# Performance work log

Measured on AMD Instinct MI355X. Metric: run time of the kernel, lower is better.

## Reference

```python
import jax, jax.numpy as jnp
import numpy as np

NUM_HEADS = 16
R_MIN = 16
R_MAX = 64


def setup_inputs() -> dict:
    key = jax.random.key(0)
    ks = jax.random.split(key, 12)
    bs, S, H = 4, 2048, 1024
    hidden_states = jax.random.normal(ks[0], (bs, S, H), dtype=jnp.float32)
    # Linear layers: y = x @ W.T + b (torch convention, W is [out, in])
    wscale = 1.0 / np.sqrt(H)
    Wq = jax.random.normal(ks[1], (H, H), dtype=jnp.float32) * wscale
    bq = jnp.zeros((H,), dtype=jnp.float32)
    Wk = jax.random.normal(ks[2], (H, H), dtype=jnp.float32) * wscale
    bk = jnp.zeros((H,), dtype=jnp.float32)
    Wv = jax.random.normal(ks[3], (H, H), dtype=jnp.float32) * wscale
    bv = jnp.zeros((H,), dtype=jnp.float32)
    Wo = jax.random.normal(ks[4], (H, H), dtype=jnp.float32) * wscale
    bo = jnp.zeros((H,), dtype=jnp.float32)
    # xavier_uniform for proj_k/proj_v over last two dims (seq_len, r_max)
    xs = float(np.sqrt(6.0 / (S + R_MAX)))
    proj_k = jax.random.uniform(ks[5], (NUM_HEADS, S, R_MAX), dtype=jnp.float32, minval=-xs, maxval=xs)
    proj_v = jax.random.uniform(ks[6], (NUM_HEADS, S, R_MAX), dtype=jnp.float32, minval=-xs, maxval=xs)
    return {
        'hidden_states': hidden_states,
        'Wq': Wq, 'bq': bq, 'Wk': Wk, 'bk': bk, 'Wv': Wv, 'bv': bv,
        'Wo': Wo, 'bo': bo, 'proj_k': proj_k, 'proj_v': proj_v,
    }


def reference(hidden_states, Wq, bq, Wk, bk, Wv, bv, Wo, bo, proj_k, proj_v):
    bs, S, H = hidden_states.shape
    nh = NUM_HEADS
    hd = H // nh

    def heads(x):  # [b,s,H] -> [b,h,s,d]
        return x.reshape(bs, S, nh, hd).transpose(0, 2, 1, 3)

    q = heads(hidden_states @ Wq.T + bq)
    k = heads(hidden_states @ Wk.T + bk)
    v = heads(hidden_states @ Wv.T + bv)

    # dynamic rank from per-sample variance (torch .var is unbiased -> ddof=1)
    batch_var = jnp.var(hidden_states.reshape(bs, -1), axis=1, ddof=1)
    var_norm = (batch_var - batch_var.min()) / (batch_var.max() - batch_var.min() + 1e-6)
    curr_r = jnp.round(R_MIN + var_norm.mean() * (R_MAX - R_MIN)).astype(jnp.int32)

    # low-rank projection of K/V along sequence; compute full r_max, mask at softmax
    key_proj = jnp.einsum('bhld,hlk->bhkd', k, proj_k)      # [b,h,R,d]
    value_proj = jnp.einsum('bhld,hlk->bhkd', v, proj_v)    # [b,h,R,d]

    scores = jnp.einsum('bhsd,bhkd->bhsk', q, key_proj) / jnp.sqrt(jnp.float32(hd))
    rank_mask = jnp.arange(R_MAX) < curr_r                  # [R]
    scores = jnp.where(rank_mask, scores, -jnp.inf)
    attn_probs = jax.nn.softmax(scores, axis=-1)            # zeros beyond curr_r
    # dropout is identity in eval mode
    context = jnp.einsum('bhsk,bhkd->bhsd', attn_probs, value_proj)
    context = context.transpose(0, 2, 1, 3).reshape(bs, S, H)
    output = context @ Wo.T + bo
    return output, attn_probs, curr_r
```

## Files before the change

kernel.cpp:

```cpp
#include <hip/hip_runtime.h>


typedef unsigned short u16;
typedef short s16x8 __attribute__((ext_vector_type(8)));
typedef unsigned short u16x8 __attribute__((ext_vector_type(8)));
typedef float f32x4 __attribute__((ext_vector_type(4)));

#define GLL16(gp, lp) __builtin_amdgcn_global_load_lds( \
    (const __attribute__((address_space(1))) void*)(gp), \
    (__attribute__((address_space(3))) void*)(lp), 16, 0, 0)

__device__ __forceinline__ u16 f2bf(float f) {
    unsigned u = __float_as_uint(f);
    u += 0x7fffu + ((u >> 16) & 1u);
    return (u16)(u >> 16);
}

__device__ __forceinline__ f32x4 mfma16(s16x8 a, s16x8 b, f32x4 c) {
    return __builtin_amdgcn_mfma_f32_16x16x32_bf16(a, b, c, 0, 0, 0);
}

__global__ __launch_bounds__(256) void cast_hs_var_k(const float* __restrict__ hs,
        u16* __restrict__ out, double* __restrict__ red) {
    int t = threadIdx.x;
    size_t base = (size_t)blockIdx.x * 8192;
    double s = 0.0, s2 = 0.0;
    #pragma unroll
    for (int i = 0; i < 4; ++i) {
        size_t idx = base + (size_t)i * 2048 + (size_t)t * 8;
        float4 a = *(const float4*)(hs + idx);
        float4 c = *(const float4*)(hs + idx + 4);
        s  += (double)a.x + (double)a.y + (double)a.z + (double)a.w
            + (double)c.x + (double)c.y + (double)c.z + (double)c.w;
        s2 += (double)a.x * a.x + (double)a.y * a.y + (double)a.z * a.z + (double)a.w * a.w
            + (double)c.x * c.x + (double)c.y * c.y + (double)c.z * c.z + (double)c.w * c.w;
        u16x8 o;
        o[0] = f2bf(a.x); o[1] = f2bf(a.y); o[2] = f2bf(a.z); o[3] = f2bf(a.w);
        o[4] = f2bf(c.x); o[5] = f2bf(c.y); o[6] = f2bf(c.z); o[7] = f2bf(c.w);
        *(u16x8*)(out + idx) = o;
    }
    __shared__ double sa[256], sb[256];
    sa[t] = s; sb[t] = s2;
    __syncthreads();
    for (int o = 128; o > 0; o >>= 1) {
        if (t < o) { sa[t] += sa[t + o]; sb[t] += sb[t + o]; }
        __syncthreads();
    }
    if (t == 0) { red[blockIdx.x * 2] = sa[0]; red[blockIdx.x * 2 + 1] = sb[0]; }
}

__global__ __launch_bounds__(256) void compute_r_k(const double* __restrict__ red,
        int* __restrict__ currp, float* __restrict__ outr) {
    int t = threadIdx.x, lane = t & 63, b = t >> 6;
    double s = 0.0, s2 = 0.0;
    #pragma unroll
    for (int j = 0; j < 4; ++j) {
        int idx = b * 256 + j * 64 + lane;
        s += red[idx * 2]; s2 += red[idx * 2 + 1];
    }
    #pragma unroll
    for (int o = 1; o < 64; o <<= 1) { s += __shfl_xor(s, o); s2 += __shfl_xor(s2, o); }
    __shared__ double vs[4];
    if (lane == 0) {
        const double N = 2097152.0;
        vs[b] = (s2 - s * s / N) / (N - 1.0);
    }
    __syncthreads();
    if (t == 0) {
        double mn = vs[0], mx = vs[0];
        for (int i = 1; i < 4; ++i) { mn = fmin(mn, vs[i]); mx = fmax(mx, vs[i]); }
        double mean = 0.0;
        for (int i = 0; i < 4; ++i) mean += (vs[i] - mn) / (mx - mn + 1e-6);
        mean *= 0.25;
        double r = rint(16.0 + mean * 48.0);
        *currp = (int)r;
        *outr = (float)r;
    }
}

__global__ __launch_bounds__(256) void prep_k(const float* __restrict__ w0,
        const float* __restrict__ w1, const float* __restrict__ w2,
        const float* __restrict__ w3, u16* __restrict__ wout,
        const float* __restrict__ p0, const float* __restrict__ p1,
        u16* __restrict__ q0, u16* __restrict__ q1,
        const float* __restrict__ bq, const float* __restrict__ bk,
        const float* __restrict__ bv, float* __restrict__ biascat) {
    __shared__ float tl[64][65];
    int bid = blockIdx.x, t = threadIdx.x;
    if (bid < 2048) {
        int mat = bid >> 9;
        int off = ((bid & 511) * 256 + t) * 8;
        const float* src = (mat == 0) ? w0 : (mat == 1) ? w1 : (mat == 2) ? w2 : w3;
        float4 a = *(const float4*)(src + off);
        float4 c = *(const float4*)(src + off + 4);
        u16x8 o;
        o[0] = f2bf(a.x); o[1] = f2bf(a.y); o[2] = f2bf(a.z); o[3] = f2bf(a.w);
        o[4] = f2bf(c.x); o[5] = f2bf(c.y); o[6] = f2bf(c.z); o[7] = f2bf(c.w);
        *(u16x8*)(wout + (size_t)mat * 1048576 + off) = o;
    } else if (bid < 3072) {
        int bid2 = bid - 2048;
        int which = bid2 >> 9, bi = bid2 & 511;
        const float* p = which ? p1 : p0;
        u16* pt = which ? q1 : q0;
        int h = bi >> 5, lb = bi & 31;
        {
            int l = t >> 2, r0 = (t & 3) * 16;
            const float* src = p + ((size_t)(h * 2048 + lb * 64 + l)) * 64 + r0;
            #pragma unroll
            for (int u = 0; u < 4; ++u) {
                float4 v = *(const float4*)(src + u * 4);
                tl[l][r0 + u * 4 + 0] = v.x; tl[l][r0 + u * 4 + 1] = v.y;
                tl[l][r0 + u * 4 + 2] = v.z; tl[l][r0 + u * 4 + 3] = v.w;
            }
        }
        __syncthreads();
        {
            int r = t >> 2, l0 = (t & 3) * 16;
            u16x8 o0, o1;
            #pragma unroll
            for (int j = 0; j < 8; ++j) { o0[j] = f2bf(tl[l0 + j][r]); o1[j] = f2bf(tl[l0 + 8 + j][r]); }
            u16* dst = pt + ((size_t)(h * 64 + r)) * 2048 + lb * 64 + l0;
            *(u16x8*)dst = o0;
            *(u16x8*)(dst + 8) = o1;
        }
    } else {
        for (int i = t; i < 3072; i += 256) {
            float v = (i < 1024) ? bq[i] : (i < 2048) ? bk[i - 1024] : bv[i - 2048];
            biascat[i] = v;
        }
    }
}

__global__ __launch_bounds__(512, 2) void qkv_gemm_k(const u16* __restrict__ Ag,
        const u16* __restrict__ Wcat, const float* __restrict__ biascat,
        u16* __restrict__ C) {
    __shared__ u16 lds[40960];
    int bid = blockIdx.x;
    int swz = (bid & 7) * 32 + (bid >> 3);
    int bm = swz >> 3, bn = swz & 7;
    int t = threadIdx.x, lane = t & 63, w = t >> 6, wr = w >> 2, wc = w & 3;

    int srow = w * 16 + (lane >> 2);
    int slog = (((lane & 3) ^ ((lane >> 3) & 3)) << 3);
    const u16* asrc0 = Ag + (size_t)(bm * 256 + srow) * 1024 + slog;
    const u16* bsrc0 = Wcat + (size_t)(bn * 384 + srow) * 1024 + slog;

#define STAGEA(kts, h) GLL16(asrc0 + (h) * 131072 + (kts) * 32, \
                             &lds[(((kts) & 1) * 8192) + (h) * 4096 + w * 512])
#define STAGEB(kts, h) GLL16(bsrc0 + (h) * 131072 + (kts) * 32, \
                             &lds[16384 + (((kts) & 1) * 12288) + (h) * 4096 + w * 512])

    int pcol = (((lane >> 4) ^ (((lane & 15) >> 1) & 3)) << 3);
    int arow0 = (wr * 128 + (lane & 15)) * 32 + pcol;
    int brow0 = 16384 + (wc * 96 + (lane & 15)) * 32 + pcol;

    f32x4 zero4 = {0.f, 0.f, 0.f, 0.f};
    f32x4 acc[8][6];
    #pragma unroll
    for (int m = 0; m < 8; ++m)
        #pragma unroll
        for (int n = 0; n < 6; ++n) acc[m][n] = zero4;

    STAGEA(0, 0); STAGEA(0, 1); STAGEB(0, 0); STAGEB(0, 1); STAGEB(0, 2);
    STAGEA(1, 0); STAGEA(1, 1);
    asm volatile("s_waitcnt vmcnt(2)" ::: "memory");
    __builtin_amdgcn_s_barrier();
    asm volatile("" ::: "memory");

    for (int kt = 0; kt < 32; ++kt) {
        int abase = (kt & 1) * 8192 + arow0;
        int bbase = (kt & 1) * 12288 + brow0;
        s16x8 af[8], bf0, bf1, bf2;

        #pragma unroll
        for (int m = 0; m < 8; ++m) af[m] = *(const s16x8*)&lds[abase + m * 512];
        bf0 = *(const s16x8*)&lds[bbase];
        bf1 = *(const s16x8*)&lds[bbase + 512];
        bf2 = *(const s16x8*)&lds[bbase + 1024];
        if (kt < 31) { STAGEB(kt + 1, 0); STAGEB(kt + 1, 1); STAGEB(kt + 1, 2); }
        asm volatile("s_waitcnt lgkmcnt(0)" ::: "memory");
        __builtin_amdgcn_s_barrier();
        __builtin_amdgcn_s_setprio(1);
        #pragma unroll
        for (int m = 0; m < 8; ++m) {
            acc[m][0] = mfma16(af[m], bf0, acc[m][0]);
            acc[m][1] = mfma16(af[m], bf1, acc[m][1]);
            acc[m][2] = mfma16(af[m], bf2, acc[m][2]);
        }
        __builtin_amdgcn_s_setprio(0);
        __builtin_amdgcn_s_barrier();
        asm volatile("" ::: "memory");

        bf0 = *(const s16x8*)&lds[bbase + 1536];
        bf1 = *(const s16x8*)&lds[bbase + 2048];
        bf2 = *(const s16x8*)&lds[bbase + 2560];
        if (kt < 30) { STAGEA(kt + 2, 0); STAGEA(kt + 2, 1); }
        if (kt < 30) { asm volatile("s_waitcnt vmcnt(2)" ::: "memory"); }
        else if (kt == 30) { asm volatile("s_waitcnt vmcnt(0)" ::: "memory"); }
        asm volatile("s_waitcnt lgkmcnt(0)" ::: "memory");
        __builtin_amdgcn_s_barrier();
        __builtin_amdgcn_s_setprio(1);
        #pragma unroll
        for (int m = 0; m < 8; ++m) {
            acc[m][3] = mfma16(af[m], bf0, acc[m][3]);
            acc[m][4] = mfma16(af[m], bf1, acc[m][4]);
            acc[m][5] = mfma16(af[m], bf2, acc[m][5]);
        }
        __builtin_amdgcn_s_setprio(0);
        __builtin_amdgcn_s_barrier();
        asm volatile("" ::: "memory");
    }

    float bias[6];
    #pragma unroll
    for (int n = 0; n < 6; ++n)
        bias[n] = biascat[bn * 384 + wc * 96 + n * 16 + (lane & 15)];
    #pragma unroll
    for (int m = 0; m < 8; ++m) {
        int row0 = bm * 256 + wr * 128 + m * 16 + ((lane >> 4) << 2);
        #pragma unroll
        for (int n = 0; n < 6; ++n) {
            int col = bn * 384 + wc * 96 + n * 16 + (lane & 15);
            #pragma unroll
            for (int v = 0; v < 4; ++v)
                C[(size_t)(row0 + v) * 3072 + col] = f2bf(acc[m][n][v] + bias[n]);
        }
    }
#undef STAGEA
#undef STAGEB
}

__global__ __launch_bounds__(512, 2) void out_gemm_k(const u16* __restrict__ Ag,
        const u16* __restrict__ Bg, const float* __restrict__ biasg,
        float* __restrict__ Cg) {
    __shared__ u16 lds[24576];
    int bid = blockIdx.x;
    int swz = (bid & 7) * 32 + (bid >> 3);
    int bm = swz >> 3, bn = swz & 7;
    int t = threadIdx.x, lane = t & 63, w = t >> 6, wr = w >> 1, wc = w & 1;

    int srow = w * 16 + (lane >> 2);
    int slog = (((lane & 3) ^ ((lane >> 3) & 3)) << 3);
    const u16* asrc0 = Ag + (size_t)(bm * 256 + srow) * 1024 + slog;
    const u16* bsrc0 = Bg + (size_t)(bn * 128 + srow) * 1024 + slog;

#define STAGEA(kts, h) GLL16(asrc0 + (h) * 131072 + (kts) * 32, \
                             &lds[(((kts) & 1) * 8192) + (h) * 4096 + w * 512])
#define STAGEB(kts) GLL16(bsrc0 + (kts) * 32, \
                          &lds[16384 + (((kts) & 1) * 4096) + w * 512])

    int pcol = (((lane >> 4) ^ (((lane & 15) >> 1) & 3)) << 3);
    int arow0 = (wr * 64 + (lane & 15)) * 32 + pcol;
    int brow0 = 16384 + (wc * 64 + (lane & 15)) * 32 + pcol;

    f32x4 zero4 = {0.f, 0.f, 0.f, 0.f};
    f32x4 acc[4][4];
    #pragma unroll
    for (int m = 0; m < 4; ++m)
        #pragma unroll
        for (int n = 0; n < 4; ++n) acc[m][n] = zero4;

    STAGEA(0, 0); STAGEA(0, 1); STAGEB(0);
    STAGEA(1, 0); STAGEA(1, 1);
    asm volatile("s_waitcnt vmcnt(2)" ::: "memory");
    __builtin_amdgcn_s_barrier();
    asm volatile("" ::: "memory");

    for (int kt = 0; kt < 32; ++kt) {
        int abase = (kt & 1) * 8192 + arow0;
        int bbase = (kt & 1) * 4096 + brow0;
        s16x8 af[4], bf0, bf1;

        #pragma unroll
        for (int m = 0; m < 4; ++m) af[m] = *(const s16x8*)&lds[abase + m * 512];
        bf0 = *(const s16x8*)&lds[bbase];
        bf1 = *(const s16x8*)&lds[bbase + 512];
        if (kt < 31) STAGEB(kt + 1);
        asm volatile("s_waitcnt lgkmcnt(0)" ::: "memory");
        __builtin_amdgcn_s_barrier();
        __builtin_amdgcn_s_setprio(1);
        #pragma unroll
        for (int m = 0; m < 4; ++m) {
            acc[m][0] = mfma16(af[m], bf0, acc[m][0]);
            acc[m][1] = mfma16(af[m], bf1, acc[m][1]);
        }
        __builtin_amdgcn_s_setprio(0);
        __builtin_amdgcn_s_barrier();
        asm volatile("" ::: "memory");

        bf0 = *(const s16x8*)&lds[bbase + 1024];
        bf1 = *(const s16x8*)&lds[bbase + 1536];
        if (kt < 30) { STAGEA(kt + 2, 0); STAGEA(kt + 2, 1); }
        if (kt < 30) { asm volatile("s_waitcnt vmcnt(2)" ::: "memory"); }
        else if (kt == 30) { asm volatile("s_waitcnt vmcnt(0)" ::: "memory"); }
        asm volatile("s_waitcnt lgkmcnt(0)" ::: "memory");
        __builtin_amdgcn_s_barrier();
        __builtin_amdgcn_s_setprio(1);
        #pragma unroll
        for (int m = 0; m < 4; ++m) {
            acc[m][2] = mfma16(af[m], bf0, acc[m][2]);
            acc[m][3] = mfma16(af[m], bf1, acc[m][3]);
        }
        __builtin_amdgcn_s_setprio(0);
        __builtin_amdgcn_s_barrier();
        asm volatile("" ::: "memory");
    }

    float bias[4];
    #pragma unroll
    for (int n = 0; n < 4; ++n)
        bias[n] = biasg[bn * 128 + wc * 64 + n * 16 + (lane & 15)];
    #pragma unroll
    for (int m = 0; m < 4; ++m) {
        int row0 = bm * 256 + wr * 64 + m * 16 + ((lane >> 4) << 2);
        #pragma unroll
        for (int n = 0; n < 4; ++n) {
            int col = bn * 128 + wc * 64 + n * 16 + (lane & 15);
            #pragma unroll
            for (int v = 0; v < 4; ++v)
                Cg[(size_t)(row0 + v) * 1024 + col] = acc[m][n][v] + bias[n];
        }
    }
#undef STAGEA
#undef STAGEB
}

__global__ __launch_bounds__(256) void proj_einsum_k(const u16* __restrict__ qkv,
        const u16* __restrict__ pt0, const u16* __restrict__ pt1,
        float* __restrict__ out0, float* __restrict__ out1) {
    __shared__ u16 kt[256 * 66];
    int c = blockIdx.x, h = blockIdx.y, z = blockIdx.z;
    int which = z >> 2, b = z & 3;
    const u16* kv = qkv + 1024 + which * 1024;
    const u16* pt = which ? pt1 : pt0;
    float* outp = which ? out1 : out0;
    int t = threadIdx.x, lane = t & 63, w = t >> 6;

    int tl = t >> 3, sd = (t & 7) * 8;
    const u16* kvp = kv + (size_t)(b * 2048 + c * 256 + tl) * 3072 + h * 64 + sd;
    s16x8 g[8];
    #pragma unroll
    for (int i = 0; i < 8; ++i) g[i] = *(const s16x8*)(kvp + (size_t)i * 98304);
    #pragma unroll
    for (int i = 0; i < 8; ++i) *(s16x8*)&kt[(tl + 32 * i) * 66 + sd] = g[i];
    __syncthreads();

    f32x4 zero4 = {0.f, 0.f, 0.f, 0.f};
    f32x4 acc[4] = {zero4, zero4, zero4, zero4};
    const u16* ptb_ = pt + (size_t)(h * 64 + (lane & 15)) * 2048 + c * 256 + ((lane >> 4) << 3);
    int gcol = w * 16 + (lane & 15);
    int gk0 = (lane >> 4) << 3;

    #pragma unroll
    for (int ks = 0; ks < 8; ++ks) {
        s16x8 bf;
        int kb = (ks * 32 + gk0) * 66 + gcol;
        #pragma unroll
        for (int j = 0; j < 8; ++j) bf[j] = (short)kt[kb + j * 66];
        #pragma unroll
        for (int m = 0; m < 4; ++m) {
            s16x8 af = *(const s16x8*)(ptb_ + (size_t)m * 32768 + ks * 32);
            acc[m] = mfma16(af, bf, acc[m]);
        }
    }

    float* ob = outp + (size_t)((c * 4 + b) * 16 + h) * 4096;
    #pragma unroll
    for (int m = 0; m < 4; ++m)
        #pragma unroll
        for (int v = 0; v < 4; ++v)
            ob[(m * 16 + ((lane >> 4) << 2) + v) * 64 + w * 16 + (lane & 15)] = acc[m][v];
}

__global__ __launch_bounds__(256) void reduce_kv_k(const float* __restrict__ kp_part,
        const float* __restrict__ vp_part, u16* __restrict__ kpb, u16* __restrict__ vpb) {
    int h = blockIdx.x, b = blockIdx.y, t = threadIdx.x;
    int base = (b * 16 + h) * 4096 + t * 16;
    float4 zf = {0.f, 0.f, 0.f, 0.f};
    float4 sk[4] = {zf, zf, zf, zf}, sv[4] = {zf, zf, zf, zf};
    #pragma unroll
    for (int c = 0; c < 8; ++c) {
        #pragma unroll
        for (int u = 0; u < 4; ++u) {
            float4 a = *(const float4*)&kp_part[c * 262144 + base + u * 4];
            float4 g = *(const float4*)&vp_part[c * 262144 + base + u * 4];
            sk[u].x += a.x; sk[u].y += a.y; sk[u].z += a.z; sk[u].w += a.w;
            sv[u].x += g.x; sv[u].y += g.y; sv[u].z += g.z; sv[u].w += g.w;
        }
    }
    int r = t >> 2, d0 = (t & 3) * 16;
    size_t ob = (size_t)(b * 16 + h) * 4096;
    u16x8 o0, o1;
    o0[0] = f2bf(sk[0].x); o0[1] = f2bf(sk[0].y); o0[2] = f2bf(sk[0].z); o0[3] = f2bf(sk[0].w);
    o0[4] = f2bf(sk[1].x); o0[5] = f2bf(sk[1].y); o0[6] = f2bf(sk[1].z); o0[7] = f2bf(sk[1].w);
    o1[0] = f2bf(sk[2].x); o1[1] = f2bf(sk[2].y); o1[2] = f2bf(sk[2].z); o1[3] = f2bf(sk[2].w);
    o1[4] = f2bf(sk[3].x); o1[5] = f2bf(sk[3].y); o1[6] = f2bf(sk[3].z); o1[7] = f2bf(sk[3].w);
    *(u16x8*)&kpb[ob + r * 64 + d0]     = o0;
    *(u16x8*)&kpb[ob + r * 64 + d0 + 8] = o1;
    #pragma unroll
    for (int u = 0; u < 4; ++u) {
        int d = d0 + u * 4;
        vpb[ob + (size_t)(d + 0) * 64 + r] = f2bf(sv[u].x);
        vpb[ob + (size_t)(d + 1) * 64 + r] = f2bf(sv[u].y);
        vpb[ob + (size_t)(d + 2) * 64 + r] = f2bf(sv[u].z);
        vpb[ob + (size_t)(d + 3) * 64 + r] = f2bf(sv[u].w);
    }
}

__global__ __launch_bounds__(256) void attn_k(const u16* __restrict__ qkv,
        const u16* __restrict__ kpb, const u16* __restrict__ vpb,
        const int* __restrict__ currp, float* __restrict__ probs, u16* __restrict__ ctxb) {
    int sb = blockIdx.x, h = blockIdx.y, b = blockIdx.z;
    int cr = *currp;
    __shared__ u16 kpl[64 * 80];
    __shared__ u16 vpl[64 * 80];
    __shared__ u16 pl[64 * 80];
    int t = threadIdx.x, lane = t & 63, w = t >> 6;

    {
        int r = t >> 2, d0 = (t & 3) * 16;
        size_t ob = (size_t)(b * 16 + h) * 4096 + t * 16;
        u16x8 k0 = *(const u16x8*)(kpb + ob), k1 = *(const u16x8*)(kpb + ob + 8);
        u16x8 v0 = *(const u16x8*)(vpb + ob), v1 = *(const u16x8*)(vpb + ob + 8);
        *(u16x8*)&kpl[r * 80 + d0]     = k0;
        *(u16x8*)&kpl[r * 80 + d0 + 8] = k1;
        *(u16x8*)&vpl[r * 80 + d0]     = v0;
        *(u16x8*)&vpl[r * 80 + d0 + 8] = v1;
    }
    __syncthreads();

    const u16* qp = qkv + (size_t)(b * 2048 + sb * 64 + w * 16 + (lane & 15)) * 3072 + h * 64 + ((lane >> 4) << 3);
    s16x8 q0 = *(const s16x8*)qp;
    s16x8 q1 = *(const s16x8*)(qp + 32);
    f32x4 zero4 = {0.f, 0.f, 0.f, 0.f};
    f32x4 sc[4];
    #pragma unroll
    for (int j = 0; j < 4; ++j) {
        sc[j] = zero4;
        s16x8 k0 = *(const s16x8*)&kpl[(j * 16 + (lane & 15)) * 80 + ((lane >> 4) << 3)];
        s16x8 k1 = *(const s16x8*)&kpl[(j * 16 + (lane & 15)) * 80 + 32 + ((lane >> 4) << 3)];
        sc[j] = mfma16(q0, k0, sc[j]);
        sc[j] = mfma16(q1, k1, sc[j]);
    }

    const float scale = 0.125f;
    float p_[4][4];
    #pragma unroll
    for (int v = 0; v < 4; ++v) {
        float m = -3.0e38f;
        #pragma unroll
        for (int j = 0; j < 4; ++j) {
            int rr = j * 16 + (lane & 15);
            if (rr < cr) m = fmaxf(m, sc[j][v] * scale);
        }
        m = fmaxf(m, __shfl_xor(m, 1));
        m = fmaxf(m, __shfl_xor(m, 2));
        m = fmaxf(m, __shfl_xor(m, 4));
        m = fmaxf(m, __shfl_xor(m, 8));
        float s = 0.f;
        #pragma unroll
        for (int j = 0; j < 4; ++j) {
            int rr = j * 16 + (lane & 15);
            float p = (rr < cr) ? __expf(sc[j][v] * scale - m) : 0.f;
            p_[j][v] = p; s += p;
        }
        s += __shfl_xor(s, 1); s += __shfl_xor(s, 2);
        s += __shfl_xor(s, 4); s += __shfl_xor(s, 8);
        float inv = 1.f / s;
        #pragma unroll
        for (int j = 0; j < 4; ++j) p_[j][v] *= inv;
    }

    int srow = w * 16 + ((lane >> 4) << 2);
    #pragma unroll
    for (int v = 0; v < 4; ++v) {
        int sg = sb * 64 + srow + v;
        #pragma unroll
        for (int j = 0; j < 4; ++j) {
            int rr = j * 16 + (lane & 15);
            probs[(size_t)((b * 16 + h) * 2048 + sg) * 64 + rr] = p_[j][v];
            pl[(srow + v) * 80 + rr] = f2bf(p_[j][v]);
        }
    }
    __syncthreads();

    f32x4 co[4] = {zero4, zero4, zero4, zero4};
    #pragma unroll
    for (int ks = 0; ks < 2; ++ks) {
        s16x8 pa = *(const s16x8*)&pl[(w * 16 + (lane & 15)) * 80 + ks * 32 + ((lane >> 4) << 3)];
        #pragma unroll
        for (int n = 0; n < 4; ++n) {
            s16x8 vf = *(const s16x8*)&vpl[(n * 16 + (lane & 15)) * 80 + ks * 32 + ((lane >> 4) << 3)];
            co[n] = mfma16(pa, vf, co[n]);
        }
    }
    #pragma unroll
    for (int n = 0; n < 4; ++n)
        #pragma unroll
        for (int v = 0; v < 4; ++v)
            ctxb[(size_t)((b * 2048 + sb * 64 + srow + v) * 16 + h) * 64 + n * 16 + (lane & 15)] = f2bf(co[n][v]);
}

extern "C" void kernel_launch(void* const* d_in, const int* in_sizes, int n_in,
                              void* d_out, int out_size, void* d_ws, size_t ws_size,
                              hipStream_t stream) {
    const float* hs = (const float*)d_in[0];
    const float* Wq = (const float*)d_in[1];
    const float* bq = (const float*)d_in[2];
    const float* Wk = (const float*)d_in[3];
    const float* bk = (const float*)d_in[4];
    const float* Wv = (const float*)d_in[5];
    const float* bv = (const float*)d_in[6];
    const float* Wo = (const float*)d_in[7];
    const float* bo = (const float*)d_in[8];
    const float* pk = (const float*)d_in[9];
    const float* pv = (const float*)d_in[10];
    float* out = (float*)d_out;
    char* w = (char*)d_ws;

    u16* hsb   = (u16*)(w + 0);
    float* vp_part = (float*)(w + 0);
    u16* ctxb  = (u16*)(w + 0);
    u16* wqb   = (u16*)(w + 16777216);
    u16* ptb   = (u16*)(w + 25165824);
    u16* pvtb  = (u16*)(w + 29360128);
    u16* qkvb  = (u16*)(w + 33554432);
    float* kp_part = (float*)(w + 83886080);
    float* biascat = (float*)(w + 92274688);
    double* red    = (double*)(w + 92291072);
    int* currp     = (int*)(w + 92307456);
    u16* kpb   = (u16*)(w + 92307520);
    u16* vpb   = (u16*)(w + 92831808);

    cast_hs_var_k<<<1024, 256, 0, stream>>>(hs, hsb, red);
    compute_r_k<<<1, 256, 0, stream>>>(red, currp, out + 16777216);
    prep_k<<<3073, 256, 0, stream>>>(Wq, Wk, Wv, Wo, wqb, pk, pv, ptb, pvtb,
                                     bq, bk, bv, biascat);

    qkv_gemm_k<<<256, 512, 0, stream>>>(hsb, wqb, biascat, qkvb);

    proj_einsum_k<<<dim3(8, 16, 8), 256, 0, stream>>>(qkvb, ptb, pvtb, kp_part, vp_part);
    reduce_kv_k<<<dim3(16, 4), 256, 0, stream>>>(kp_part, vp_part, kpb, vpb);

    attn_k<<<dim3(32, 16, 4), 256, 0, stream>>>(qkvb, kpb, vpb, currp,
                                                out + 8388608, ctxb);

    out_gemm_k<<<256, 512, 0, stream>>>(ctxb, wqb + 3145728, bo, out);
}
```

Measured before the change: 154.8 us.

## Retile QKV GEMM to 256x192 blocks with BK=64 and 8-way swizzled LDS

```diff
diff --git a/kernel.cpp b/kernel.cpp
--- a/kernel.cpp
+++ b/kernel.cpp
@@ -134,50 +134,53 @@
 __global__ __launch_bounds__(512, 2) void qkv_gemm_k(const u16* __restrict__ Ag,
         const u16* __restrict__ Wcat, const float* __restrict__ biascat,
         u16* __restrict__ C) {
-    __shared__ u16 lds[40960];
+    __shared__ u16 lds[57344];
     int bid = blockIdx.x;
-    int swz = (bid & 7) * 32 + (bid >> 3);
-    int bm = swz >> 3, bn = swz & 7;
+    int swz = (bid & 7) * 64 + (bid >> 3);
+    int bm = swz >> 4, bn = swz & 15;
     int t = threadIdx.x, lane = t & 63, w = t >> 6, wr = w >> 2, wc = w & 3;
 
-    int srow = w * 16 + (lane >> 2);
-    int slog = (((lane & 3) ^ ((lane >> 3) & 3)) << 3);
-    const u16* asrc0 = Ag + (size_t)(bm * 256 + srow) * 1024 + slog;
-    const u16* bsrc0 = Wcat + (size_t)(bn * 384 + srow) * 1024 + slog;
-
-#define STAGEA(kts, h) GLL16(asrc0 + (h) * 131072 + (kts) * 32, \
-                             &lds[(((kts) & 1) * 8192) + (h) * 4096 + w * 512])
-#define STAGEB(kts, h) GLL16(bsrc0 + (h) * 131072 + (kts) * 32, \
-                             &lds[16384 + (((kts) & 1) * 12288) + (h) * 4096 + w * 512])
-
-    int pcol = (((lane >> 4) ^ (((lane & 15) >> 1) & 3)) << 3);
-    int arow0 = (wr * 128 + (lane & 15)) * 32 + pcol;
-    int brow0 = 16384 + (wc * 96 + (lane & 15)) * 32 + pcol;
+    int slog = (((lane & 7) ^ ((lane >> 3) & 7)) << 3);
+    const u16* asrc0 = Ag + (size_t)(bm * 256 + w * 32 + (lane >> 3)) * 1024 + slog;
+    const u16* bsrc0 = Wcat + (size_t)(bn * 192 + w * 24 + (lane >> 3)) * 1024 + slog;
+
+#define STAGEA(kts, h) GLL16(asrc0 + (h) * 8192 + (kts) * 64, \
+                             &lds[(((kts) & 1) * 16384) + w * 2048 + (h) * 512])
+#define STAGEB(kts, h) GLL16(bsrc0 + (h) * 8192 + (kts) * 64, \
+                             &lds[32768 + (((kts) & 1) * 12288) + w * 1536 + (h) * 512])
+
+    int li = lane & 15;
+    int arow0 = (wr * 128 + li) * 64;
+    int brow0 = 32768 + (wc * 48 + li) * 64;
+    int x0 = (((lane >> 4) + 0) ^ (lane & 7)) << 3;
+    int x1 = (((lane >> 4) + 4) ^ (lane & 7)) << 3;
 
     f32x4 zero4 = {0.f, 0.f, 0.f, 0.f};
-    f32x4 acc[8][6];
+    f32x4 acc[8][3];
     #pragma unroll
     for (int m = 0; m < 8; ++m)
         #pragma unroll
-        for (int n = 0; n < 6; ++n) acc[m][n] = zero4;
-
-    STAGEA(0, 0); STAGEA(0, 1); STAGEB(0, 0); STAGEB(0, 1); STAGEB(0, 2);
-    STAGEA(1, 0); STAGEA(1, 1);
-    asm volatile("s_waitcnt vmcnt(2)" ::: "memory");
+        for (int n = 0; n < 3; ++n) acc[m][n] = zero4;
+
+    STAGEA(0, 0); STAGEA(0, 1); STAGEA(0, 2); STAGEA(0, 3);
+    STAGEB(0, 0); STAGEB(0, 1); STAGEB(0, 2);
+    STAGEA(1, 0); STAGEA(1, 1); STAGEA(1, 2); STAGEA(1, 3);
+    STAGEB(1, 0); STAGEB(1, 1); STAGEB(1, 2);
+    asm volatile("s_waitcnt vmcnt(7)" ::: "memory");
     __builtin_amdgcn_s_barrier();
     asm volatile("" ::: "memory");
 
-    for (int kt = 0; kt < 32; ++kt) {
-        int abase = (kt & 1) * 8192 + arow0;
-        int bbase = (kt & 1) * 12288 + brow0;
+    for (int kt = 0; kt < 16; ++kt) {
+        int ab = (kt & 1) * 16384 + arow0;
+        int bb = (kt & 1) * 12288 + brow0;
         s16x8 af[8], bf0, bf1, bf2;
 
         #pragma unroll
-        for (int m = 0; m < 8; ++m) af[m] = *(const s16x8*)&lds[abase + m * 512];
-        bf0 = *(const s16x8*)&lds[bbase];
-        bf1 = *(const s16x8*)&lds[bbase + 512];
-        bf2 = *(const s16x8*)&lds[bbase + 1024];
-        if (kt < 31) { STAGEB(kt + 1, 0); STAGEB(kt + 1, 1); STAGEB(kt + 1, 2); }
+        for (int m = 0; m < 8; ++m) af[m] = *(const s16x8*)&lds[ab + m * 1024 + x0];
+        bf0 = *(const s16x8*)&lds[bb + x0];
+        bf1 = *(const s16x8*)&lds[bb + 1024 + x0];
+        bf2 = *(const s16x8*)&lds[bb + 2048 + x0];
+        if (kt < 15) { STAGEB(kt + 1, 0); STAGEB(kt + 1, 1); STAGEB(kt + 1, 2); }
         asm volatile("s_waitcnt lgkmcnt(0)" ::: "memory");
         __builtin_amdgcn_s_barrier();
         __builtin_amdgcn_s_setprio(1);
@@ -191,36 +194,38 @@
         __builtin_amdgcn_s_barrier();
         asm volatile("" ::: "memory");
 
-        bf0 = *(const s16x8*)&lds[bbase + 1536];
-        bf1 = *(const s16x8*)&lds[bbase + 2048];
-        bf2 = *(const s16x8*)&lds[bbase + 2560];
-        if (kt < 30) { STAGEA(kt + 2, 0); STAGEA(kt + 2, 1); }
-        if (kt < 30) { asm volatile("s_waitcnt vmcnt(2)" ::: "memory"); }
-        else if (kt == 30) { asm volatile("s_waitcnt vmcnt(0)" ::: "memory"); }
+        #pragma unroll
+        for (int m = 0; m < 8; ++m) af[m] = *(const s16x8*)&lds[ab + m * 1024 + x1];
+        bf0 = *(const s16x8*)&lds[bb + x1];
+        bf1 = *(const s16x8*)&lds[bb + 1024 + x1];
+        bf2 = *(const s16x8*)&lds[bb + 2048 + x1];
         asm volatile("s_waitcnt lgkmcnt(0)" ::: "memory");
         __builtin_amdgcn_s_barrier();
+        if (kt < 14) { STAGEA(kt + 2, 0); STAGEA(kt + 2, 1); STAGEA(kt + 2, 2); STAGEA(kt + 2, 3); }
         __builtin_amdgcn_s_setprio(1);
         #pragma unroll
         for (int m = 0; m < 8; ++m) {
-            acc[m][3] = mfma16(af[m], bf0, acc[m][3]);
-            acc[m][4] = mfma16(af[m], bf1, acc[m][4]);
-            acc[m][5] = mfma16(af[m], bf2, acc[m][5]);
+            acc[m][0] = mfma16(af[m], bf0, acc[m][0]);
+            acc[m][1] = mfma16(af[m], bf1, acc[m][1]);
+            acc[m][2] = mfma16(af[m], bf2, acc[m][2]);
         }
         __builtin_amdgcn_s_setprio(0);
+        if (kt < 14) { asm volatile("s_waitcnt vmcnt(4)" ::: "memory"); }
+        else if (kt == 14) { asm volatile("s_waitcnt vmcnt(0)" ::: "memory"); }
         __builtin_amdgcn_s_barrier();
         asm volatile("" ::: "memory");
     }
 
-    float bias[6];
-    #pragma unroll
-    for (int n = 0; n < 6; ++n)
-        bias[n] = biascat[bn * 384 + wc * 96 + n * 16 + (lane & 15)];
+    float bias[3];
+    #pragma unroll
+    for (int n = 0; n < 3; ++n)
+        bias[n] = biascat[bn * 192 + wc * 48 + n * 16 + li];
     #pragma unroll
     for (int m = 0; m < 8; ++m) {
         int row0 = bm * 256 + wr * 128 + m * 16 + ((lane >> 4) << 2);
         #pragma unroll
-        for (int n = 0; n < 6; ++n) {
-            int col = bn * 384 + wc * 96 + n * 16 + (lane & 15);
+        for (int n = 0; n < 3; ++n) {
+            int col = bn * 192 + wc * 48 + n * 16 + li;
             #pragma unroll
             for (int v = 0; v < 4; ++v)
                 C[(size_t)(row0 + v) * 3072 + col] = f2bf(acc[m][n][v] + bias[n]);
@@ -537,7 +542,7 @@
     prep_k<<<3073, 256, 0, stream>>>(Wq, Wk, Wv, Wo, wqb, pk, pv, ptb, pvtb,
                                      bq, bk, bv, biascat);
 
-    qkv_gemm_k<<<256, 512, 0, stream>>>(hsb, wqb, biascat, qkvb);
+    qkv_gemm_k<<<512, 512, 0, stream>>>(hsb, wqb, biascat, qkvb);
 
     proj_einsum_k<<<dim3(8, 16, 8), 256, 0, stream>>>(qkvb, ptb, pvtb, kp_part, vp_part);
     reduce_kv_k<<<dim3(16, 4), 256, 0, stream>>>(kp_part, vp_part, kpb, vpb);
```

Result: faster. 151.1 us (-2.4%).
